# Kernel tuning notes

Measured on AMD Instinct MI355X. Metric: run time of the kernel, lower is better.

Reference implementation:

```python
import jax, jax.numpy as jnp
import numpy as np

STRIDE = 16
NUM_A = 9
POS_TH, NEG_TH = 0.7, 0.3
FG, BG, IGN = 1.0, 0.0, 2.0
CAP = 128  # BATCH_SIZE * 0.5 for both fg and bg


def _generate_base_anchors(base_size=16, ratios=(0.5, 1.0, 2.0), scales=(8, 16, 32)):
    w = h = float(base_size)
    xc = yc = 0.5 * (base_size - 1)
    size = w * h
    out = []
    for r in ratios:
        ws = np.round(np.sqrt(size / r))
        hs = np.round(ws * r)
        for s in scales:
            W, H = ws * s, hs * s
            out.append([xc - 0.5 * (W - 1), yc - 0.5 * (H - 1),
                        xc + 0.5 * (W - 1), yc + 0.5 * (H - 1)])
    return np.asarray(out, dtype=np.float32)  # [9,4]


def _all_anchors(H, W):
    base = _generate_base_anchors()
    sx = np.arange(W, dtype=np.float32) * STRIDE
    sy = np.arange(H, dtype=np.float32) * STRIDE
    xs, ys = np.meshgrid(sx, sy)  # row-major over (h, w)
    shifts = np.stack([xs.ravel(), ys.ravel(), xs.ravel(), ys.ravel()], 1)
    return jnp.asarray((shifts[:, None, :] + base[None, :, :]).reshape(-1, 4))  # [H*W*9,4], order (h,w,a)


def _forward(scores, gt, im_w, im_h):
    H, W = scores.shape[2], scores.shape[3]
    anchors = _all_anchors(H, W)  # [N,4]
    valid = (anchors[:, 0] >= 0.) & (anchors[:, 1] >= 0.) & \
            (anchors[:, 2] < im_w) & (anchors[:, 3] < im_h)
    # pairwise IoU with +1 box convention
    aw = anchors[:, 2] - anchors[:, 0] + 1.
    ah = anchors[:, 3] - anchors[:, 1] + 1.
    a_area = jnp.where((aw > 0) & (ah > 0), aw * ah, 0.)
    gw = gt[:, 2] - gt[:, 0] + 1.
    gh = gt[:, 3] - gt[:, 1] + 1.
    g_area = jnp.where((gw > 0) & (gh > 0), gw * gh, 0.)
    ix1 = jnp.maximum(anchors[:, None, 0], gt[None, :, 0])
    iy1 = jnp.maximum(anchors[:, None, 1], gt[None, :, 1])
    ix2 = jnp.minimum(anchors[:, None, 2], gt[None, :, 2])
    iy2 = jnp.minimum(anchors[:, None, 3], gt[None, :, 3])
    iw = ix2 - ix1 + 1.
    ih = iy2 - iy1 + 1.
    inter = jnp.where((iw > 0) & (ih > 0), iw * ih, 0.)
    ovl = inter / (a_area[:, None] + g_area[None, :] - inter)  # [N,G]
    ovl_m = jnp.where(valid[:, None], ovl, -1.)  # exclude invalid anchors
    a_argmax = jnp.argmax(ovl, axis=1)           # best gt per anchor
    a_max = jnp.max(ovl, axis=1)
    g_max = jnp.max(ovl_m, axis=0)               # best (valid) anchor overlap per gt
    gt_fg = jnp.any(ovl_m == g_max[None, :], axis=1) & valid
    labels = jnp.where(valid & (a_max < NEG_TH), BG, IGN)
    labels = jnp.where(gt_fg, FG, labels)
    labels = jnp.where(valid & (a_max >= POS_TH), FG, labels)
    # random subsample fg/bg down to CAP each (matches npr.choice semantics in distribution)
    kf, kb = jax.random.split(jax.random.key(42))
    def subsample(lbl, mask, k):
        s = jnp.where(mask, jax.random.uniform(k, lbl.shape), jnp.inf)
        ranks = jnp.argsort(jnp.argsort(s))
        keep = ranks < jnp.minimum(jnp.sum(mask), CAP)
        return jnp.where(mask & ~keep, IGN, lbl)
    labels = subsample(labels, labels == FG, kf)
    labels = subsample(labels, labels == BG, kb)
    num_ni = jnp.sum(labels != IGN).astype(jnp.float32)
    gts = gt[a_argmax]
    ax = (anchors[:, 2] + anchors[:, 0]) * 0.5
    ay = (anchors[:, 3] + anchors[:, 1]) * 0.5
    gwm = gts[:, 2] - gts[:, 0] + 1.
    ghm = gts[:, 3] - gts[:, 1] + 1.
    gx = (gts[:, 2] + gts[:, 0]) * 0.5
    gy = (gts[:, 3] + gts[:, 1]) * 0.5
    adj = jnp.stack([(gx - ax) / aw, (gy - ay) / ah,
                     jnp.log(gwm / aw), jnp.log(ghm / ah)], axis=1)  # [N,4]
    adj = jnp.where(valid[:, None], adj, 0.)
    wts = jnp.where((labels == FG)[:, None], 1.0 / num_ni, 0.) * jnp.ones((1, 4), jnp.float32)
    labels_out = labels.reshape(1, H, W, NUM_A).transpose(0, 3, 1, 2) \
                       .reshape(1, 1, NUM_A * H, W).astype(jnp.int32)
    adj_out = adj.reshape(1, H, W, 4 * NUM_A).transpose(0, 3, 1, 2)
    wts_out = wts.reshape(1, H, W, 4 * NUM_A).transpose(0, 3, 1, 2)
    return labels_out, adj_out, wts_out


def setup_inputs() -> dict:
    key = jax.random.key(0)
    k1, k2, k3 = jax.random.split(key, 3)
    scores = jax.random.normal(k1, (1, 18, 256, 256), dtype=jnp.float32)
    G = 64
    cxy = jax.random.uniform(k2, (G, 2), minval=100., maxval=3900.)
    wh = jax.random.uniform(k3, (G, 2), minval=32., maxval=512.)
    x1y1 = jnp.clip(cxy - wh * 0.5, 0., 4095.)
    x2y2 = jnp.clip(cxy + wh * 0.5, 0., 4095.)
    gt = jnp.concatenate([x1y1, x2y2], axis=1)  # [G,4] = x1,y1,x2,y2
    return {"anchor_object_scores": scores, "ground_truth_boxes": gt,
            "im_w": 4096, "im_h": 4096}


def reference(anchor_object_scores, ground_truth_boxes, im_w, im_h):
    return _forward(anchor_object_scores, ground_truth_boxes, im_w, im_h)
```

## Files before the change

kernel.cpp:

```cpp
#include <hip/hip_runtime.h>
#include <stdint.h>


#define NUM_A 9
#define HW 65536
#define N_ANCH 589824
#define NG 64
#define CAPK 128u
#define NBIN 2048
#define BIN_SHIFT 12
#define CAND_CAP 2048

#define LAB_BG 0u
#define LAB_FG 1u
#define LAB_IGN 2u

#define NBLK 576

#define OFF_HF    0
#define OFF_HB    NBIN
#define OFF_CNTF  (2*NBIN)
#define OFF_CNTB  (OFF_CNTF + 1)
#define OFF_ROOTB (OFF_CNTF + 2)
#define OFF_ROOTD (OFF_CNTF + 3)
#define OFF_SEL   4104
#define OFF_SUBB  4112
#define OFF_SUBD  (OFF_SUBB + 32*16)
#define OFF_CFLG  (OFF_SUBD + 32*16)
#define CTRL_WORDS (OFF_CFLG + 32*16)
#define OFF_CANDF CTRL_WORDS
#define OFF_CANDB (OFF_CANDF + 2*CAND_CAP)

#define MAGIC_C 0x5CA1AB1Eu

__constant__ float BA[NUM_A][4] = {
  { -84.f,  -40.f,  99.f,  55.f}, {-176.f,  -88.f, 191.f, 103.f},
  {-360.f, -184.f, 375.f, 199.f}, { -56.f,  -56.f,  71.f,  71.f},
  {-120.f, -120.f, 135.f, 135.f}, {-248.f, -248.f, 263.f, 263.f},
  { -36.f,  -80.f,  51.f,  95.f}, { -80.f, -168.f,  95.f, 183.f},
  {-168.f, -344.f, 183.f, 359.f}};

__host__ __device__ static inline void tf2x32(uint32_t k0, uint32_t k1,
                                              uint32_t x0, uint32_t x1,
                                              uint32_t* o0, uint32_t* o1) {
  const uint32_t ks2 = k0 ^ k1 ^ 0x1BD11BDAu;
#define TF_R(r) { x0 += x1; x1 = (x1 << (r)) | (x1 >> (32 - (r))); x1 ^= x0; }
  x0 += k0; x1 += k1;
  TF_R(13) TF_R(15) TF_R(26) TF_R(6)
  x0 += k1;  x1 += ks2 + 1u;
  TF_R(17) TF_R(29) TF_R(16) TF_R(24)
  x0 += ks2; x1 += k0 + 2u;
  TF_R(13) TF_R(15) TF_R(26) TF_R(6)
  x0 += k0;  x1 += k1 + 3u;
  TF_R(17) TF_R(29) TF_R(16) TF_R(24)
  x0 += k1;  x1 += ks2 + 4u;
  TF_R(13) TF_R(15) TF_R(26) TF_R(6)
  x0 += ks2; x1 += k0 + 5u;
#undef TF_R
  *o0 = x0; *o1 = x1;
}

__device__ static inline uint32_t mant_of(uint32_t k0, uint32_t k1, uint32_t n) {
  uint32_t o0, o1;
  tf2x32(k0, k1, 0u, n, &o0, &o1);
  return (o0 ^ o1) >> 9;
}

__device__ static inline float axis_best(float blo, float bhi, float glo,
                                         float ghi, int lo, int hi) {
  #pragma clang fp contract(off)
  float t1 = (ghi - bhi) * 0.0625f;
  float t2 = (glo - blo) * 0.0625f;
  float tmin = fminf(t1, t2), tmax = fmaxf(t1, t2);
  int c1 = (int)floorf(tmin), c2 = (int)ceilf(tmax);
  int cand0 = lo, cand1 = hi;
  int cand2 = min(max(c1,     lo), hi);
  int cand3 = min(max(c1 + 1, lo), hi);
  int cand4 = min(max(c2 - 1, lo), hi);
  int cand5 = min(max(c2,     lo), hi);
  float best = -3.0e38f;
  int cands[6] = {cand0, cand1, cand2, cand3, cand4, cand5};
  #pragma unroll
  for (int i = 0; i < 6; i++) {
    float s = (float)(cands[i] << 4);
    float v = fminf(bhi + s, ghi) - fmaxf(blo + s, glo) + 1.0f;
    best = fmaxf(best, v);
  }
  return best;
}

#define AG_LOAD(p)      __hip_atomic_load((p), __ATOMIC_RELAXED, __HIP_MEMORY_SCOPE_AGENT)
#define AG_STORE(p, v)  __hip_atomic_store((p), (v), __ATOMIC_RELAXED, __HIP_MEMORY_SCOPE_AGENT)

__global__ __launch_bounds__(256) void k_one(const float* __restrict__ gt,
                                             const int* __restrict__ imw_p,
                                             const int* __restrict__ imh_p,
                                             float* __restrict__ out_lab,
                                             float* __restrict__ out_adj,
                                             float* __restrict__ out_wts,
                                             uint32_t* __restrict__ ws,
                                             uint32_t kf0, uint32_t kf1,
                                             uint32_t kb0, uint32_t kb1) {
  #pragma clang fp contract(off)
  __shared__ float sg0[NG], sg1[NG], sg2[NG], sg3[NG], sga[NG], sgm[NG];
  __shared__ uint32_t sgmU[NG];
  __shared__ uint32_t sh[2 * NBIN];
  __shared__ unsigned long long sMask[4];
  __shared__ int sAnyZero, sLastB, sLastD;
  __shared__ uint32_t sSel[8];
  int tid = threadIdx.x;
  int b = blockIdx.x;
  int a = b >> 6, hb = (b & 63) << 2;

  {
    uint4* sh4 = (uint4*)sh;
    #pragma unroll
    for (int k = 0; k < 4; k++) sh4[tid + k * 256] = make_uint4(0, 0, 0, 0);
  }
  if (tid == 0) sAnyZero = 0;
  if (tid < NG) {
    const float4 g4 = ((const float4*)gt)[tid];
    sg0[tid] = g4.x; sg1[tid] = g4.y; sg2[tid] = g4.z; sg3[tid] = g4.w;
    float gw = g4.z - g4.x + 1.0f, gh = g4.w - g4.y + 1.0f;
    sga[tid] = (gw > 0.0f && gh > 0.0f) ? gw * gh : 0.0f;
    sgmU[tid] = 0u;
  }
  __syncthreads();

  {
    int imwi = imw_p[0], imhi = imh_p[0];
    for (int p = tid; p < NG * NUM_A; p += 256) {
      int g = p / NUM_A, q = p - g * NUM_A;
      float b0 = BA[q][0], b1 = BA[q][1], b2 = BA[q][2], b3 = BA[q][3];
      int ib0 = (int)b0, ib1 = (int)b1, ib2 = (int)b2, ib3 = (int)b3;
      int wlo = max(0, (-ib0 + 15) >> 4);
      int whi = min(255, (imwi - ib2 - 1) >> 4);
      int hlo = max(0, (-ib1 + 15) >> 4);
      int hhi = min(255, (imhi - ib3 - 1) >> 4);
      if (wlo > whi || hlo > hhi) continue;
      float iwb = axis_best(b0, b2, sg0[g], sg2[g], wlo, whi);
      float ihb = axis_best(b1, b3, sg1[g], sg3[g], hlo, hhi);
      float aw = b2 - b0 + 1.0f, ah = b3 - b1 + 1.0f;
      float aarea = aw * ah;
      float inter = (iwb > 0.0f && ihb > 0.0f) ? iwb * ihb : 0.0f;
      float den = aarea + sga[g] - inter;
      float o = inter / den;
      atomicMax(&sgmU[g], __float_as_uint(o));
    }
  }

  {
    int wv = tid >> 6, g = tid & 63;
    float sy = (float)((hb + wv) << 4);
    float ihp = fminf(BA[a][3] + sy, sg3[g]) - fmaxf(BA[a][1] + sy, sg1[g]) + 1.0f;
    unsigned long long mk = __ballot(ihp > 0.0f);
    if (g == 0) sMask[wv] = mk;
  }
  __syncthreads();
  if (tid < NG) {
    uint32_t mm = sgmU[tid];
    sgm[tid] = __uint_as_float(mm);
    if (mm == 0u) atomicOr(&sAnyZero, 1);
  }
  __syncthreads();

  float BA0 = BA[a][0], BA1 = BA[a][1], BA2 = BA[a][2], BA3 = BA[a][3];
  float imw = (float)imw_p[0], imh = (float)imh_p[0];
  int w = tid;
  float sx = (float)(w << 4);
  float A0 = BA0 + sx, A2 = BA2 + sx;
  float aw = A2 - A0 + 1.0f;
  float A1v[4], A3v[4];
  #pragma unroll
  for (int r = 0; r < 4; r++) {
    float sy = (float)((hb + r) << 4);
    A1v[r] = BA1 + sy; A3v[r] = BA3 + sy;
  }
  float ah = A3v[0] - A1v[0] + 1.0f;
  float aarea = aw * ah;
  bool xv = (A0 >= 0.0f) && (A2 < imw);

  unsigned long long mk0 = sMask[0], mk1 = sMask[1],
                     mk2 = sMask[2], mk3 = sMask[3];
  unsigned long long uni = mk0 | mk1 | mk2 | mk3;
  float amaxv[4] = {0.f, 0.f, 0.f, 0.f};
  int bgv[4] = {0, 0, 0, 0};
  uint32_t afv = 0u;
  while (uni) {
    int g = __ffsll(uni) - 1;
    uni &= uni - 1;
    float iw = fminf(A2, sg2[g]) - fmaxf(A0, sg0[g]) + 1.0f;
    if (!__any(iw > 0.0f)) continue;
    if (iw > 0.0f) {
      float base = aarea + sga[g];
      float gy1 = sg1[g], gy2 = sg3[g], gm = sgm[g];
#define DO_ROW(r, mk)                                                     \
      if ((mk >> g) & 1ull) {                                             \
        float ih = fminf(A3v[r], gy2) - fmaxf(A1v[r], gy1) + 1.0f;        \
        float inter = iw * ih;                                            \
        float o = inter / (base - inter);                                 \
        if (o > amaxv[r]) { amaxv[r] = o; bgv[r] = g; }                   \
        if (o == gm) afv |= (1u << r);                                    \
      }
      DO_ROW(0, mk0) DO_ROW(1, mk1) DO_ROW(2, mk2) DO_ROW(3, mk3)
#undef DO_ROW
    }
  }

  bool anyZ = (sAnyZero != 0);
  uint32_t lm[4];
  #pragma unroll
  for (int r = 0; r < 4; r++) {
    int hw = (hb + r) * 256 + w;
    bool valid = xv && (A1v[r] >= 0.0f) && (A3v[r] < imh);
    float amax = amaxv[r];
    bool anyfg = (((afv >> r) & 1u) || anyZ) && valid;
    uint32_t lab;
    if (!valid)                       lab = LAB_IGN;
    else if (anyfg || amax >= 0.7f)   lab = LAB_FG;
    else if (amax < 0.3f)             lab = LAB_BG;
    else                              lab = LAB_IGN;

    float adj0 = 0.f, adj1 = 0.f, adj2 = 0.f, adj3 = 0.f;
    if (valid) {
      int bg = bgv[r];
      float G0 = sg0[bg], G1 = sg1[bg], G2 = sg2[bg], G3 = sg3[bg];
      float ax = (A2 + A0) * 0.5f, ay = (A3v[r] + A1v[r]) * 0.5f;
      float gwm = G2 - G0 + 1.0f, ghm = G3 - G1 + 1.0f;
      float gx = (G2 + G0) * 0.5f, gy = (G3 + G1) * 0.5f;
      adj0 = (gx - ax) / aw;
      adj1 = (gy - ay) / ah;
      adj2 = logf(gwm / aw);
      adj3 = logf(ghm / ah);
    }
    int c4 = a * 4;
    out_adj[(c4 + 0) * HW + hw] = adj0;
    out_adj[(c4 + 1) * HW + hw] = adj1;
    out_adj[(c4 + 2) * HW + hw] = adj2;
    out_adj[(c4 + 3) * HW + hw] = adj3;

    uint32_t m = 0u;
    uint32_t n = (uint32_t)(hw * 9 + a);
    if (lab != LAB_IGN) {
      uint32_t kk0 = (lab == LAB_FG) ? kf0 : kb0;
      uint32_t kk1 = (lab == LAB_FG) ? kf1 : kb1;
      m = mant_of(kk0, kk1, n);
      atomicAdd(&sh[((lab == LAB_FG) ? 0 : NBIN) + (m >> BIN_SHIFT)], 1u);
    }
    lm[r] = (lab << 24) | m;
  }
  __syncthreads();

  for (int i = tid; i < 2 * NBIN; i += 256) {
    uint32_t v = sh[i];
    if (v) atomicAdd(&ws[OFF_HF + i], v);
  }
  asm volatile("s_waitcnt vmcnt(0)" ::: "memory");
  __syncthreads();

  if (tid == 0) {
    int last = 0;
    uint32_t v = atomicAdd(&ws[OFF_SUBB + (b & 31) * 16], 1u);
    if (v == 17u) {
      uint32_t r = atomicAdd(&ws[OFF_ROOTB], 1u);
      if (r == 31u) last = 1;
    }
    sLastB = last;
  }
  __syncthreads();
  if (sLastB) {
    for (int cls = 0; cls < 2; cls++) {
      uint32_t* hist = ws + (cls ? OFF_HB : OFF_HF);
      uint32_t* sel = ws + OFF_SEL + cls * 4;
      uint32_t loc[8], s = 0;
      #pragma unroll
      for (int j = 0; j < 8; j++) {
        loc[j] = AG_LOAD(&hist[tid * 8 + j]);
        s += loc[j];
      }
      sh[tid] = s; __syncthreads();
      for (int off = 1; off < 256; off <<= 1) {
        uint32_t v = (tid >= off) ? sh[tid - off] : 0u;
        __syncthreads();
        sh[tid] += v;
        __syncthreads();
      }
      uint32_t total = sh[255];
      uint32_t K = total < CAPK ? total : CAPK;
      if (tid == 0) {
        AG_STORE(&sel[3], K);
        if (K == 0u) {
          AG_STORE(&sel[0], 0xFFFFFFFFu); AG_STORE(&sel[1], 0u);
          AG_STORE(&sel[2], 0u);
        }
      }
      if (K > 0u) {
        uint32_t myC = sh[tid], pvC = (tid == 0) ? 0u : sh[tid - 1];
        if (myC >= K && pvC < K) {
          uint32_t cum = pvC; int bb = tid * 8;
          for (int j = 0; j < 8; j++) {
            if (cum + loc[j] >= K) { bb = tid * 8 + j; break; }
            cum += loc[j];
          }
          AG_STORE(&sel[0], (uint32_t)bb); AG_STORE(&sel[1], cum);
          AG_STORE(&sel[2], K - cum);
        }
      }
      __syncthreads();
    }
    asm volatile("s_waitcnt vmcnt(0)" ::: "memory");
    __syncthreads();
    if (tid < 32) AG_STORE(&ws[OFF_CFLG + tid * 16], MAGIC_C);
  }

  if (tid == 0) {
    while (AG_LOAD(&ws[OFF_CFLG + (b & 31) * 16]) != MAGIC_C)
      __builtin_amdgcn_s_sleep(2);
  }
  __syncthreads();
  if (tid < 8) sSel[tid] = AG_LOAD(&ws[OFF_SEL + tid]);
  __syncthreads();
  uint32_t bf = sSel[0], Kf = sSel[3], bbn = sSel[4], Kb = sSel[7];
  float inv = 1.0f / (float)(Kf + Kb);

  #pragma unroll
  for (int r = 0; r < 4; r++) {
    int hw = (hb + r) * 256 + w;
    uint32_t lab = lm[r] >> 24;
    uint32_t m = lm[r] & 0x7FFFFFu;
    uint32_t n = (uint32_t)(hw * 9 + a);
    float outv = 2.0f, wv = 0.0f;
    bool skip = false;
    if (lab == LAB_FG) {
      uint32_t bn = m >> BIN_SHIFT;
      if (bn < bf) { outv = 1.0f; wv = inv; }
      else if (bn == bf) {
        uint32_t idx = atomicAdd(&ws[OFF_CNTF], 1u);
        if (idx < CAND_CAP) {
          AG_STORE((uint64_t*)(ws + OFF_CANDF) + idx,
                   ((uint64_t)m << 20) | (uint64_t)n);
          skip = true;
        }
      }
    } else if (lab == LAB_BG) {
      uint32_t bn = m >> BIN_SHIFT;
      if (bn < bbn) { outv = 0.0f; }
      else if (bn == bbn) {
        uint32_t idx = atomicAdd(&ws[OFF_CNTB], 1u);
        if (idx < CAND_CAP) {
          AG_STORE((uint64_t*)(ws + OFF_CANDB) + idx,
                   ((uint64_t)m << 20) | (uint64_t)n);
          skip = true;
        }
      }
    }
    if (!skip) {
      out_lab[a * HW + hw] = outv;
      int c4 = a * 4;
      out_wts[(c4 + 0) * HW + hw] = wv;
      out_wts[(c4 + 1) * HW + hw] = wv;
      out_wts[(c4 + 2) * HW + hw] = wv;
      out_wts[(c4 + 3) * HW + hw] = wv;
    }
  }

  asm volatile("s_waitcnt vmcnt(0)" ::: "memory");
  __syncthreads();

  if (tid == 0) {
    int last = 0;
    uint32_t v = atomicAdd(&ws[OFF_SUBD + (b & 31) * 16], 1u);
    if (v == 17u) {
      uint32_t r = atomicAdd(&ws[OFF_ROOTD], 1u);
      if (r == 31u) last = 1;
    }
    sLastD = last;
  }
  __syncthreads();
  if (sLastD) {
    uint64_t* sc = (uint64_t*)sh;
    for (int cls = 0; cls < 2; cls++) {
      uint32_t cnt = AG_LOAD(&ws[cls == 0 ? OFF_CNTF : OFF_CNTB]);
      uint32_t C = cnt < CAND_CAP ? cnt : CAND_CAP;
      uint32_t need = AG_LOAD(&ws[OFF_SEL + cls * 4 + 2]);
      const uint64_t* cand =
          (const uint64_t*)(ws + (cls == 0 ? OFF_CANDF : OFF_CANDB));
      for (uint32_t i = tid; i < C; i += 256) sc[i] = AG_LOAD(&cand[i]);
      __syncthreads();
      for (uint32_t i = tid; i < C; i += 256) {
        uint64_t k = sc[i];
        uint32_t rr = 0;
        for (uint32_t j = 0; j < C; j++) rr += (sc[j] < k) ? 1u : 0u;
        bool kept = (rr < need);
        uint32_t nn = (uint32_t)(k & 0xFFFFFu);
        uint32_t aa = nn % 9u, hww = nn / 9u;
        uint32_t tt = aa * HW + hww;
        float lv = kept ? (cls == 0 ? 1.0f : 0.0f) : 2.0f;
        float wvv = (kept && cls == 0) ? inv : 0.0f;
        AG_STORE(&out_lab[tt], lv);
        #pragma unroll
        for (int j2 = 0; j2 < 4; j2++)
          AG_STORE(&out_wts[(aa * 4 + j2) * HW + hww], wvv);
      }
      __syncthreads();
    }
  }
}

extern "C" void kernel_launch(void* const* d_in, const int* in_sizes, int n_in,
                              void* d_out, int out_size, void* d_ws,
                              size_t ws_size, hipStream_t stream) {
  const float* gt  = (const float*)d_in[1];
  const int*   imw = (const int*)d_in[2];
  const int*   imh = (const int*)d_in[3];
  float* out      = (float*)d_out;
  float* out_lab  = out;
  float* out_adj  = out + N_ANCH;
  float* out_wts  = out + 5 * N_ANCH;
  uint32_t* ws = (uint32_t*)d_ws;

  uint32_t kf0, kf1, kb0, kb1;
  tf2x32(0u, 42u, 0u, 0u, &kf0, &kf1);
  tf2x32(0u, 42u, 0u, 1u, &kb0, &kb1);

  hipMemsetAsync(ws, 0, CTRL_WORDS * sizeof(uint32_t), stream);
  hipLaunchKernelGGL(k_one, dim3(NBLK), dim3(256), 0, stream, gt, imw, imh,
                     out_lab, out_adj, out_wts, ws, kf0, kf1, kb0, kb1);
}
```

Measured before the change: 98.77 us.

## Shrink histogram bins, shard candidate lists per group, defer final output writes

```diff
diff --git a/kernel.cpp b/kernel.cpp
--- a/kernel.cpp
+++ b/kernel.cpp
@@ -7,9 +7,11 @@
 #define N_ANCH 589824
 #define NG 64
 #define CAPK 128u
-#define NBIN 2048
-#define BIN_SHIFT 12
-#define CAND_CAP 2048
+#define NBIN 512
+#define BIN_SHIFT 14
+#define CLIST_CAP 128u
+#define NGRP 32
+#define GATHER_CAP 2048u
 
 #define LAB_BG 0u
 #define LAB_FG 1u
@@ -19,17 +21,17 @@
 
 #define OFF_HF    0
 #define OFF_HB    NBIN
-#define OFF_CNTF  (2*NBIN)
-#define OFF_CNTB  (OFF_CNTF + 1)
-#define OFF_ROOTB (OFF_CNTF + 2)
-#define OFF_ROOTD (OFF_CNTF + 3)
-#define OFF_SEL   4104
-#define OFF_SUBB  4112
+#define OFF_ROOTB (2*NBIN)
+#define OFF_ROOTD (2*NBIN + 1)
+#define OFF_SEL   1032
+#define OFF_SUBB  1040
 #define OFF_SUBD  (OFF_SUBB + 32*16)
 #define OFF_CFLG  (OFF_SUBD + 32*16)
-#define CTRL_WORDS (OFF_CFLG + 32*16)
+#define OFF_CCNTF (OFF_CFLG + 32*16)
+#define OFF_CCNTB (OFF_CCNTF + 32*16)
+#define CTRL_WORDS (OFF_CCNTB + 32*16)
 #define OFF_CANDF CTRL_WORDS
-#define OFF_CANDB (OFF_CANDF + 2*CAND_CAP)
+#define OFF_CANDB (OFF_CANDF + 2*NGRP*CLIST_CAP)
 
 #define MAGIC_C 0x5CA1AB1Eu
 
@@ -102,9 +104,10 @@
                                              uint32_t kf0, uint32_t kf1,
                                              uint32_t kb0, uint32_t kb1) {
   #pragma clang fp contract(off)
+  __shared__ uint64_t scB[GATHER_CAP];
+  uint32_t* sh = (uint32_t*)scB;
   __shared__ float sg0[NG], sg1[NG], sg2[NG], sg3[NG], sga[NG], sgm[NG];
   __shared__ uint32_t sgmU[NG];
-  __shared__ uint32_t sh[2 * NBIN];
   __shared__ unsigned long long sMask[4];
   __shared__ int sAnyZero, sLastB, sLastD;
   __shared__ uint32_t sSel[8];
@@ -112,11 +115,7 @@
   int b = blockIdx.x;
   int a = b >> 6, hb = (b & 63) << 2;
 
-  {
-    uint4* sh4 = (uint4*)sh;
-    #pragma unroll
-    for (int k = 0; k < 4; k++) sh4[tid + k * 256] = make_uint4(0, 0, 0, 0);
-  }
+  ((uint4*)sh)[tid] = make_uint4(0, 0, 0, 0);
   if (tid == 0) sAnyZero = 0;
   if (tid < NG) {
     const float4 g4 = ((const float4*)gt)[tid];
@@ -272,10 +271,10 @@
     for (int cls = 0; cls < 2; cls++) {
       uint32_t* hist = ws + (cls ? OFF_HB : OFF_HF);
       uint32_t* sel = ws + OFF_SEL + cls * 4;
-      uint32_t loc[8], s = 0;
+      uint32_t loc[2], s = 0;
       #pragma unroll
-      for (int j = 0; j < 8; j++) {
-        loc[j] = AG_LOAD(&hist[tid * 8 + j]);
+      for (int j = 0; j < 2; j++) {
+        loc[j] = AG_LOAD(&hist[tid * 2 + j]);
         s += loc[j];
       }
       sh[tid] = s; __syncthreads();
@@ -297,9 +296,10 @@
       if (K > 0u) {
         uint32_t myC = sh[tid], pvC = (tid == 0) ? 0u : sh[tid - 1];
         if (myC >= K && pvC < K) {
-          uint32_t cum = pvC; int bb = tid * 8;
-          for (int j = 0; j < 8; j++) {
-            if (cum + loc[j] >= K) { bb = tid * 8 + j; break; }
+          uint32_t cum = pvC; int bb = tid * 2;
+          #pragma unroll
+          for (int j = 0; j < 2; j++) {
+            if (cum + loc[j] >= K) { bb = tid * 2 + j; break; }
             cum += loc[j];
           }
           AG_STORE(&sel[0], (uint32_t)bb); AG_STORE(&sel[1], cum);
@@ -323,47 +323,29 @@
   uint32_t bf = sSel[0], Kf = sSel[3], bbn = sSel[4], Kb = sSel[7];
   float inv = 1.0f / (float)(Kf + Kb);
 
+  uint32_t pushedMask = 0u;
   #pragma unroll
   for (int r = 0; r < 4; r++) {
-    int hw = (hb + r) * 256 + w;
     uint32_t lab = lm[r] >> 24;
+    if (lab == LAB_IGN) continue;
     uint32_t m = lm[r] & 0x7FFFFFu;
-    uint32_t n = (uint32_t)(hw * 9 + a);
-    float outv = 2.0f, wv = 0.0f;
-    bool skip = false;
-    if (lab == LAB_FG) {
-      uint32_t bn = m >> BIN_SHIFT;
-      if (bn < bf) { outv = 1.0f; wv = inv; }
-      else if (bn == bf) {
-        uint32_t idx = atomicAdd(&ws[OFF_CNTF], 1u);
-        if (idx < CAND_CAP) {
-          AG_STORE((uint64_t*)(ws + OFF_CANDF) + idx,
-                   ((uint64_t)m << 20) | (uint64_t)n);
-          skip = true;
-        }
-      }
-    } else if (lab == LAB_BG) {
-      uint32_t bn = m >> BIN_SHIFT;
-      if (bn < bbn) { outv = 0.0f; }
-      else if (bn == bbn) {
-        uint32_t idx = atomicAdd(&ws[OFF_CNTB], 1u);
-        if (idx < CAND_CAP) {
-          AG_STORE((uint64_t*)(ws + OFF_CANDB) + idx,
-                   ((uint64_t)m << 20) | (uint64_t)n);
-          skip = true;
-        }
-      }
-    }
-    if (!skip) {
-      out_lab[a * HW + hw] = outv;
-      int c4 = a * 4;
-      out_wts[(c4 + 0) * HW + hw] = wv;
-      out_wts[(c4 + 1) * HW + hw] = wv;
-      out_wts[(c4 + 2) * HW + hw] = wv;
-      out_wts[(c4 + 3) * HW + hw] = wv;
-    }
-  }
-
+    uint32_t bn = m >> BIN_SHIFT;
+    uint32_t bnd = (lab == LAB_FG) ? bf : bbn;
+    if (bn == bnd) {
+      int hw = (hb + r) * 256 + w;
+      uint32_t n = (uint32_t)(hw * 9 + a);
+      uint32_t grp = (uint32_t)(b & 31);
+      uint32_t cbase = (lab == LAB_FG) ? OFF_CCNTF : OFF_CCNTB;
+      uint32_t idx = atomicAdd(&ws[cbase + grp * 16], 1u);
+      if (idx < CLIST_CAP) {
+        uint64_t* lst = (uint64_t*)(ws + ((lab == LAB_FG) ? OFF_CANDF
+                                                          : OFF_CANDB)) +
+                        grp * CLIST_CAP;
+        AG_STORE(&lst[idx], ((uint64_t)m << 20) | (uint64_t)n);
+        pushedMask |= (1u << r);
+      }
+    }
+  }
   asm volatile("s_waitcnt vmcnt(0)" ::: "memory");
   __syncthreads();
 
@@ -378,15 +360,23 @@
   }
   __syncthreads();
   if (sLastD) {
-    uint64_t* sc = (uint64_t*)sh;
+    uint64_t* sc = scB;
     for (int cls = 0; cls < 2; cls++) {
-      uint32_t cnt = AG_LOAD(&ws[cls == 0 ? OFF_CNTF : OFF_CNTB]);
-      uint32_t C = cnt < CAND_CAP ? cnt : CAND_CAP;
+      uint32_t total = 0;
+      for (int g2 = 0; g2 < NGRP; g2++) {
+        uint32_t cg = AG_LOAD(&ws[(cls ? OFF_CCNTB : OFF_CCNTF) + g2 * 16]);
+        cg = cg < CLIST_CAP ? cg : CLIST_CAP;
+        if (total + cg > GATHER_CAP) cg = GATHER_CAP - total;
+        const uint64_t* lst =
+            (const uint64_t*)(ws + (cls ? OFF_CANDB : OFF_CANDF)) +
+            g2 * CLIST_CAP;
+        for (uint32_t i = tid; i < cg; i += 256)
+          sc[total + i] = AG_LOAD(&lst[i]);
+        total += cg;
+      }
+      __syncthreads();
+      uint32_t C = total;
       uint32_t need = AG_LOAD(&ws[OFF_SEL + cls * 4 + 2]);
-      const uint64_t* cand =
-          (const uint64_t*)(ws + (cls == 0 ? OFF_CANDF : OFF_CANDB));
-      for (uint32_t i = tid; i < C; i += 256) sc[i] = AG_LOAD(&cand[i]);
-      __syncthreads();
       for (uint32_t i = tid; i < C; i += 256) {
         uint64_t k = sc[i];
         uint32_t rr = 0;
@@ -405,6 +395,28 @@
       __syncthreads();
     }
   }
+
+  #pragma unroll
+  for (int r = 0; r < 4; r++) {
+    if ((pushedMask >> r) & 1u) continue;
+    int hw = (hb + r) * 256 + w;
+    uint32_t lab = lm[r] >> 24;
+    uint32_t m = lm[r] & 0x7FFFFFu;
+    float outv = 2.0f, wv = 0.0f;
+    if (lab == LAB_FG) {
+      uint32_t bn = m >> BIN_SHIFT;
+      if (bn < bf) { outv = 1.0f; wv = inv; }
+    } else if (lab == LAB_BG) {
+      uint32_t bn = m >> BIN_SHIFT;
+      if (bn < bbn) outv = 0.0f;
+    }
+    out_lab[a * HW + hw] = outv;
+    int c4 = a * 4;
+    out_wts[(c4 + 0) * HW + hw] = wv;
+    out_wts[(c4 + 1) * HW + hw] = wv;
+    out_wts[(c4 + 2) * HW + hw] = wv;
+    out_wts[(c4 + 3) * HW + hw] = wv;
+  }
 }
 
 extern "C" void kernel_launch(void* const* d_in, const int* in_sizes, int n_in,
```

Result: slower. 162.2 us (+64.3%).

## Shrink selection histograms and add fast path when class count is within cap

Applied to the files above, without the earlier changes.

```diff
diff --git a/kernel.cpp b/kernel.cpp
--- a/kernel.cpp
+++ b/kernel.cpp
@@ -7,8 +7,8 @@
 #define N_ANCH 589824
 #define NG 64
 #define CAPK 128u
-#define NBIN 2048
-#define BIN_SHIFT 12
+#define NBINS 256
+#define BG_TC 65536u
 #define CAND_CAP 2048
 
 #define LAB_BG 0u
@@ -18,16 +18,18 @@
 #define NBLK 576
 
 #define OFF_HF    0
-#define OFF_HB    NBIN
-#define OFF_CNTF  (2*NBIN)
-#define OFF_CNTB  (OFF_CNTF + 1)
-#define OFF_ROOTB (OFF_CNTF + 2)
-#define OFF_ROOTD (OFF_CNTF + 3)
-#define OFF_SEL   4104
-#define OFF_SUBB  4112
-#define OFF_SUBD  (OFF_SUBB + 32*16)
-#define OFF_CFLG  (OFF_SUBD + 32*16)
-#define CTRL_WORDS (OFF_CFLG + 32*16)
+#define OFF_HB    256
+#define OFF_TOTF  512
+#define OFF_TOTB  1024
+#define OFF_SUBB  1536
+#define OFF_ROOTB 2048
+#define OFF_SUBD  2064
+#define OFF_ROOTD 2576
+#define OFF_SEL   2592
+#define OFF_CFLG  2608
+#define OFF_CNTF  3120
+#define OFF_CNTB  3136
+#define CTRL_WORDS 3152
 #define OFF_CANDF CTRL_WORDS
 #define OFF_CANDB (OFF_CANDF + 2*CAND_CAP)
 
@@ -102,22 +104,20 @@
                                              uint32_t kf0, uint32_t kf1,
                                              uint32_t kb0, uint32_t kb1) {
   #pragma clang fp contract(off)
+  __shared__ uint64_t scB[CAND_CAP];
+  uint32_t* sh = (uint32_t*)scB;
   __shared__ float sg0[NG], sg1[NG], sg2[NG], sg3[NG], sga[NG], sgm[NG];
   __shared__ uint32_t sgmU[NG];
-  __shared__ uint32_t sh[2 * NBIN];
   __shared__ unsigned long long sMask[4];
   __shared__ int sAnyZero, sLastB, sLastD;
-  __shared__ uint32_t sSel[8];
+  __shared__ uint32_t sSel[10];
+  __shared__ uint32_t sCF, sCB;
   int tid = threadIdx.x;
   int b = blockIdx.x;
   int a = b >> 6, hb = (b & 63) << 2;
 
-  {
-    uint4* sh4 = (uint4*)sh;
-    #pragma unroll
-    for (int k = 0; k < 4; k++) sh4[tid + k * 256] = make_uint4(0, 0, 0, 0);
-  }
-  if (tid == 0) sAnyZero = 0;
+  ((uint2*)sh)[tid] = make_uint2(0, 0);
+  if (tid == 0) { sAnyZero = 0; sCF = 0u; sCB = 0u; }
   if (tid < NG) {
     const float4 g4 = ((const float4*)gt)[tid];
     sg0[tid] = g4.x; sg1[tid] = g4.y; sg2[tid] = g4.z; sg3[tid] = g4.w;
@@ -209,6 +209,7 @@
 
   bool anyZ = (sAnyZero != 0);
   uint32_t lm[4];
+  uint32_t cfLoc = 0, cbLoc = 0;
   #pragma unroll
   for (int r = 0; r < 4; r++) {
     int hw = (hb + r) * 256 + w;
@@ -245,15 +246,27 @@
       uint32_t kk0 = (lab == LAB_FG) ? kf0 : kb0;
       uint32_t kk1 = (lab == LAB_FG) ? kf1 : kb1;
       m = mant_of(kk0, kk1, n);
-      atomicAdd(&sh[((lab == LAB_FG) ? 0 : NBIN) + (m >> BIN_SHIFT)], 1u);
+      if (lab == LAB_FG) {
+        cfLoc++;
+        atomicAdd(&sh[m >> 15], 1u);
+      } else {
+        cbLoc++;
+        if (m < BG_TC) atomicAdd(&sh[NBINS + (m >> 8)], 1u);
+      }
     }
     lm[r] = (lab << 24) | m;
   }
-  __syncthreads();
-
-  for (int i = tid; i < 2 * NBIN; i += 256) {
+  if (cfLoc) atomicAdd(&sCF, cfLoc);
+  if (cbLoc) atomicAdd(&sCB, cbLoc);
+  __syncthreads();
+
+  for (int i = tid; i < 2 * NBINS; i += 256) {
     uint32_t v = sh[i];
     if (v) atomicAdd(&ws[OFF_HF + i], v);
+  }
+  if (tid == 0) {
+    if (sCF) atomicAdd(&ws[OFF_TOTF + (b & 31) * 16], sCF);
+    if (sCB) atomicAdd(&ws[OFF_TOTB + (b & 31) * 16], sCB);
   }
   asm volatile("s_waitcnt vmcnt(0)" ::: "memory");
   __syncthreads();
@@ -269,41 +282,45 @@
   }
   __syncthreads();
   if (sLastB) {
+    __shared__ uint32_t sTots[64];
+    if (tid < 32)       sTots[tid] = AG_LOAD(&ws[OFF_TOTF + tid * 16]);
+    else if (tid < 64)  sTots[tid] = AG_LOAD(&ws[OFF_TOTB + (tid - 32) * 16]);
+    __syncthreads();
+    uint32_t totF = 0, totB = 0;
+    if (tid == 0) {
+      for (int i = 0; i < 32; i++) { totF += sTots[i]; totB += sTots[32 + i]; }
+      sTots[0] = totF; sTots[1] = totB;
+    }
+    __syncthreads();
+    totF = sTots[0]; totB = sTots[1];
+
     for (int cls = 0; cls < 2; cls++) {
       uint32_t* hist = ws + (cls ? OFF_HB : OFF_HF);
-      uint32_t* sel = ws + OFF_SEL + cls * 4;
-      uint32_t loc[8], s = 0;
-      #pragma unroll
-      for (int j = 0; j < 8; j++) {
-        loc[j] = AG_LOAD(&hist[tid * 8 + j]);
-        s += loc[j];
-      }
-      sh[tid] = s; __syncthreads();
+      uint32_t* sel = ws + OFF_SEL + cls * 5;
+      uint32_t tot = cls ? totB : totF;
+      uint32_t K = tot < CAPK ? tot : CAPK;
+      uint32_t loc = AG_LOAD(&hist[tid]);
+      sh[tid] = loc; __syncthreads();
       for (int off = 1; off < 256; off <<= 1) {
         uint32_t v = (tid >= off) ? sh[tid - off] : 0u;
         __syncthreads();
         sh[tid] += v;
         __syncthreads();
       }
-      uint32_t total = sh[255];
-      uint32_t K = total < CAPK ? total : CAPK;
       if (tid == 0) {
-        AG_STORE(&sel[3], K);
-        if (K == 0u) {
-          AG_STORE(&sel[0], 0xFFFFFFFFu); AG_STORE(&sel[1], 0u);
-          AG_STORE(&sel[2], 0u);
+        uint32_t mode = (K == 0u) ? 0u : ((tot <= CAPK) ? 1u : 2u);
+        AG_STORE(&sel[0], mode);
+        AG_STORE(&sel[4], K);
+        if (mode != 2u) {
+          AG_STORE(&sel[1], 0xFFFFFFFFu); AG_STORE(&sel[2], 0u);
+          AG_STORE(&sel[3], 0u);
         }
       }
-      if (K > 0u) {
+      if (K > 0u && tot > CAPK) {
         uint32_t myC = sh[tid], pvC = (tid == 0) ? 0u : sh[tid - 1];
         if (myC >= K && pvC < K) {
-          uint32_t cum = pvC; int bb = tid * 8;
-          for (int j = 0; j < 8; j++) {
-            if (cum + loc[j] >= K) { bb = tid * 8 + j; break; }
-            cum += loc[j];
-          }
-          AG_STORE(&sel[0], (uint32_t)bb); AG_STORE(&sel[1], cum);
-          AG_STORE(&sel[2], K - cum);
+          AG_STORE(&sel[1], (uint32_t)tid); AG_STORE(&sel[2], pvC);
+          AG_STORE(&sel[3], K - pvC);
         }
       }
       __syncthreads();
@@ -318,9 +335,11 @@
       __builtin_amdgcn_s_sleep(2);
   }
   __syncthreads();
-  if (tid < 8) sSel[tid] = AG_LOAD(&ws[OFF_SEL + tid]);
-  __syncthreads();
-  uint32_t bf = sSel[0], Kf = sSel[3], bbn = sSel[4], Kb = sSel[7];
+  if (tid < 10) sSel[tid] = AG_LOAD(&ws[OFF_SEL + tid]);
+  __syncthreads();
+  uint32_t mF = sSel[0], bbF = sSel[1];
+  uint32_t mB = sSel[5], bbB = sSel[6];
+  uint32_t Kf = sSel[4], Kb = sSel[9];
   float inv = 1.0f / (float)(Kf + Kb);
 
   #pragma unroll
@@ -332,25 +351,31 @@
     float outv = 2.0f, wv = 0.0f;
     bool skip = false;
     if (lab == LAB_FG) {
-      uint32_t bn = m >> BIN_SHIFT;
-      if (bn < bf) { outv = 1.0f; wv = inv; }
-      else if (bn == bf) {
-        uint32_t idx = atomicAdd(&ws[OFF_CNTF], 1u);
-        if (idx < CAND_CAP) {
-          AG_STORE((uint64_t*)(ws + OFF_CANDF) + idx,
-                   ((uint64_t)m << 20) | (uint64_t)n);
-          skip = true;
+      if (mF == 1u) { outv = 1.0f; wv = inv; }
+      else if (mF == 2u) {
+        uint32_t bn = m >> 15;
+        if (bn < bbF) { outv = 1.0f; wv = inv; }
+        else if (bn == bbF) {
+          uint32_t idx = atomicAdd(&ws[OFF_CNTF], 1u);
+          if (idx < CAND_CAP) {
+            AG_STORE((uint64_t*)(ws + OFF_CANDF) + idx,
+                     ((uint64_t)m << 20) | (uint64_t)n);
+            skip = true;
+          }
         }
       }
     } else if (lab == LAB_BG) {
-      uint32_t bn = m >> BIN_SHIFT;
-      if (bn < bbn) { outv = 0.0f; }
-      else if (bn == bbn) {
-        uint32_t idx = atomicAdd(&ws[OFF_CNTB], 1u);
-        if (idx < CAND_CAP) {
-          AG_STORE((uint64_t*)(ws + OFF_CANDB) + idx,
-                   ((uint64_t)m << 20) | (uint64_t)n);
-          skip = true;
+      if (mB == 1u) { outv = 0.0f; }
+      else if (mB == 2u && m < BG_TC) {
+        uint32_t bn = m >> 8;
+        if (bn < bbB) { outv = 0.0f; }
+        else if (bn == bbB) {
+          uint32_t idx = atomicAdd(&ws[OFF_CNTB], 1u);
+          if (idx < CAND_CAP) {
+            AG_STORE((uint64_t*)(ws + OFF_CANDB) + idx,
+                     ((uint64_t)m << 20) | (uint64_t)n);
+            skip = true;
+          }
         }
       }
     }
@@ -378,19 +403,19 @@
   }
   __syncthreads();
   if (sLastD) {
-    uint64_t* sc = (uint64_t*)sh;
     for (int cls = 0; cls < 2; cls++) {
       uint32_t cnt = AG_LOAD(&ws[cls == 0 ? OFF_CNTF : OFF_CNTB]);
       uint32_t C = cnt < CAND_CAP ? cnt : CAND_CAP;
-      uint32_t need = AG_LOAD(&ws[OFF_SEL + cls * 4 + 2]);
+      uint32_t need = AG_LOAD(&ws[OFF_SEL + cls * 5 + 3]);
       const uint64_t* cand =
           (const uint64_t*)(ws + (cls == 0 ? OFF_CANDF : OFF_CANDB));
-      for (uint32_t i = tid; i < C; i += 256) sc[i] = AG_LOAD(&cand[i]);
+      for (uint32_t i = tid; i < C; i += 256)
+        scB[i] = AG_LOAD(&cand[i]);
       __syncthreads();
       for (uint32_t i = tid; i < C; i += 256) {
-        uint64_t k = sc[i];
+        uint64_t k = scB[i];
         uint32_t rr = 0;
-        for (uint32_t j = 0; j < C; j++) rr += (sc[j] < k) ? 1u : 0u;
+        for (uint32_t j = 0; j < C; j++) rr += (scB[j] < k) ? 1u : 0u;
         bool kept = (rr < need);
         uint32_t nn = (uint32_t)(k & 0xFFFFFu);
         uint32_t aa = nn % 9u, hww = nn / 9u;
```

Measured after the change: 93.03 us. 5.8% less time.
